# Kernel tuning notes

Measured on AMD Instinct MI355X. Metric: run time of the kernel, lower is better.

## Reference

```python
import jax, jax.numpy as jnp
import numpy as np

K = 20           # top_k
EPS_NORM = 1e-12  # F.normalize default eps


def setup_inputs() -> dict:
    key = jax.random.key(0)
    ks = jax.random.split(key, 16)
    B, C, R, S, SCB, ST, H = 8192, 3755, 214, 13, 30, 6, 64
    return {
        "char_logits": jax.random.normal(ks[0], (B, C), jnp.float32),
        "radical_logits": jax.random.normal(ks[1], (B, R), jnp.float32),
        "structure": jax.random.normal(ks[2], (B, S), jnp.float32),
        "stroke_count": jax.random.normal(ks[3], (B, SCB), jnp.float32),
        "stroke_types": jax.random.normal(ks[4], (B, ST), jnp.float32),
        "radical_mask": jax.random.randint(ks[5], (C, R), 0, 2, jnp.int32),
        "structure_label": jax.random.randint(ks[6], (C,), 0, S, jnp.int32),
        "stroke_count_label": jax.random.randint(ks[7], (C,), 0, SCB, jnp.int32),
        "stroke_type_sig": jax.random.uniform(ks[8], (C, ST), jnp.float32),
        "W1": jax.random.normal(ks[9], (6, H), jnp.float32) * 0.3,
        "b1": jax.random.normal(ks[10], (H,), jnp.float32) * 0.1,
        "W2": jax.random.normal(ks[11], (H, 1), jnp.float32) * 0.3,
        "b2": jax.random.normal(ks[12], (1,), jnp.float32) * 0.1,
        "reranker_weight": jnp.asarray(0.1, jnp.float32),
    }


def _features(char_logits, radical_logits, structure, stroke_count, stroke_types,
              radical_mask, structure_label, stroke_count_label, stroke_type_sig,
              top_idx):
    sg = jax.lax.stop_gradient
    # all model outputs except char_logits are detached by caller; char_logits
    # is detached inside _compute_features for the neural-confidence feature
    rl, st, sc, sty = sg(radical_logits), sg(structure), sg(stroke_count), sg(stroke_types)
    cl_d = sg(char_logits)

    # feature 1/2: radical match & false-alarm ratios
    radical_probs = jax.nn.sigmoid(rl)                              # (B, R)
    cand_mask = radical_mask[top_idx].astype(jnp.float32)           # (B, K, R)
    detected = jnp.einsum('br,bkr->bk', radical_probs, cand_mask)   # (B, K)
    cand_counts = jnp.maximum(cand_mask.sum(-1), 1.0)
    radical_match_ratio = detected / cand_counts
    total_prob = jnp.maximum(radical_probs.sum(-1, keepdims=True), 1e-6)  # (B,1)
    false_alarm_mass = radical_probs.sum(-1, keepdims=True) - detected
    radical_false_ratio = false_alarm_mass / total_prob

    # feature 3: structure match probability
    structure_probs = jax.nn.softmax(st, axis=-1)                   # (B, S)
    cand_structure = structure_label[top_idx]                       # (B, K)
    structure_match = jnp.take_along_axis(structure_probs, cand_structure, axis=1)

    # feature 4: normalized stroke-count distance
    stroke_pred = jnp.argmax(sc, axis=-1)                           # (B,)
    cand_stroke = stroke_count_label[top_idx]                       # (B, K)
    stroke_distance = jnp.abs(stroke_pred[:, None] - cand_stroke).astype(jnp.float32) / 29.0

    # feature 5: zero-masked stroke-type cosine
    cand_sig = stroke_type_sig[top_idx]                             # (B, K, 6)
    sig_norm_val = jnp.linalg.norm(cand_sig, axis=-1)               # (B, K)
    has_sig = (sig_norm_val > 1e-6).astype(jnp.float32)
    pred_norm = sty / jnp.maximum(jnp.linalg.norm(sty, axis=-1, keepdims=True), EPS_NORM)
    cand_adj = cand_sig + 1e-8 * (1.0 - has_sig)[..., None]
    cand_norm = cand_adj / jnp.maximum(jnp.linalg.norm(cand_adj, axis=-1, keepdims=True), EPS_NORM)
    stroke_type_cos = jnp.einsum('bd,bkd->bk', pred_norm, cand_norm) * has_sig

    # feature 6: detached neural confidence
    neural_probs = jax.nn.softmax(cl_d, axis=-1)                    # (B, C)
    neural_conf = jnp.take_along_axis(neural_probs, top_idx, axis=1)

    return jnp.stack([radical_match_ratio, radical_false_ratio, structure_match,
                      stroke_distance, stroke_type_cos, neural_conf], axis=-1)  # (B, K, 6)


def reference(char_logits, radical_logits, structure, stroke_count, stroke_types,
              radical_mask, structure_label, stroke_count_label, stroke_type_sig,
              W1, b1, W2, b2, reranker_weight):
    B = char_logits.shape[0]
    top_logits, top_idx = jax.lax.top_k(char_logits, K)             # (B, K)
    feats = _features(char_logits, radical_logits, structure, stroke_count,
                      stroke_types, radical_mask, structure_label,
                      stroke_count_label, stroke_type_sig, top_idx)
    h = jax.nn.relu(feats @ W1 + b1)                                # (B, K, H)
    rerank_scores = (h @ W2 + b2)[..., 0]                           # (B, K)
    combined_top = top_logits + reranker_weight * rerank_scores
    rows = jnp.arange(B)[:, None]
    return char_logits.at[rows, top_idx].set(combined_top)
```

## Files before the change

kernel.cpp:

```cpp
#include <hip/hip_runtime.h>
#include <math.h>

#define NB   8192
#define NC   3755
#define NR   214
#define NS   13
#define NSC  30
#define NST  6
#define NH   64
#define KTOP 20
#define RPB  4
#define NT   (RPB * 64)
#define NQT  15
#define NBIN 1024
#define CAP  192

__device__ __forceinline__ unsigned sortkey(float x) {
    unsigned u = __float_as_uint(x);
    return (u & 0x80000000u) ? ~u : (u | 0x80000000u);
}
__device__ __forceinline__ float inv_sortkey(unsigned k) {
    unsigned u = (k & 0x80000000u) ? (k ^ 0x80000000u) : ~k;
    return __uint_as_float(u);
}

__global__ __launch_bounds__(NT, 8) void select_kernel(
    const float* __restrict__ char_logits,
    float*       __restrict__ out,
    float*       __restrict__ ws_topv,
    int*         __restrict__ ws_topi,
    float*       __restrict__ ws_stat)
{
    const int tid  = threadIdx.x;
    const int lane = tid & 63;
    const int wave = tid >> 6;
    const int row  = blockIdx.x * RPB + wave;

    __shared__ unsigned           s_hist32[RPB / 2][NBIN];
    __shared__ unsigned long long s_cand[RPB][CAP];
    __shared__ int s_cnt[RPB];
    __shared__ int s_need[RPB];

    const int      hw  = wave >> 1;
    const unsigned hsh = (wave & 1) * 16;

    const size_t rowOff = (size_t)row * NC;
    const float* __restrict__ rin  = char_logits + rowOff;
    float*       __restrict__ rout = out + rowOff;

    const int a     = (int)((4 - (rowOff & 3)) & 3);
    const int nq    = (NC - a) >> 2;
    const int ntail = NC - a - 4 * nq;

    int ext_idx = -1;
    if (lane < a)                           ext_idx = lane;
    else if (lane >= 8 && lane < 8 + ntail) ext_idx = a + 4 * nq + (lane - 8);

    for (int i = tid; i < (RPB / 2) * NBIN; i += NT)
        (&s_hist32[0][0])[i] = 0u;
    if (tid < RPB) s_cnt[tid] = 0;
    __syncthreads();

    const unsigned floork1 = 0xC0000000u;
    float m0 = -INFINITY, m1 = -INFINITY, m2 = -INFINITY, m3 = -INFINITY;
    float ext = -INFINITY;
    if (ext_idx >= 0) {
        ext = rin[ext_idx]; rout[ext_idx] = ext;
        unsigned k = sortkey(ext);
        if (k >= floork1) atomicAdd(&s_hist32[hw][k >> 22], 1u << hsh);
    }
    for (int t = 0; t < NQT; ++t) {
        int q = lane + t * 64;
        if (q < nq) {
            float4 x = *reinterpret_cast<const float4*>(rin + a + 4 * q);
            *reinterpret_cast<float4*>(rout + a + 4 * q) = x;
            m0 = fmaxf(m0, x.x); m1 = fmaxf(m1, x.y);
            m2 = fmaxf(m2, x.z); m3 = fmaxf(m3, x.w);
            unsigned k0 = sortkey(x.x), k1 = sortkey(x.y);
            unsigned k2 = sortkey(x.z), k3 = sortkey(x.w);
            if (k0 >= floork1) atomicAdd(&s_hist32[hw][k0 >> 22], 1u << hsh);
            if (k1 >= floork1) atomicAdd(&s_hist32[hw][k1 >> 22], 1u << hsh);
            if (k2 >= floork1) atomicAdd(&s_hist32[hw][k2 >> 22], 1u << hsh);
            if (k3 >= floork1) atomicAdd(&s_hist32[hw][k3 >> 22], 1u << hsh);
        }
    }
    float lmax = fmaxf(fmaxf(m0, m1), fmaxf(fmaxf(m2, m3), ext));
#pragma unroll
    for (int off = 32; off > 0; off >>= 1) lmax = fmaxf(lmax, __shfl_xor(lmax, off));
    const float rowmax = lmax;
    __syncthreads();

    int B0 = -1;
    {
        int bb = (int)(sortkey(rowmax) >> 22);
        int fb = (int)(floork1 >> 22);
        int cum = 0;
        while (bb >= fb) {
            cum += (int)((s_hist32[hw][bb] >> hsh) & 0xFFFFu);
            if (cum >= KTOP) break;
            --bb;
        }
        B0 = (cum >= KTOP) ? bb : -1;
    }
    const int need2 = (B0 < 0) ? 1 : 0;
    if (lane == 0) s_need[wave] = need2;
    __syncthreads();

    const int any2 = s_need[0] | s_need[1] | s_need[2] | s_need[3];
    if (any2) {
        if (need2) {
#pragma unroll
            for (int i = 0; i < NBIN / 64; ++i) s_hist32[hw][lane + i * 64] = 0u;
        }
        __syncthreads();
        if (need2) {
            for (int t = 0; t < NQT; ++t) {
                int q = lane + t * 64;
                if (q < nq) {
                    float4 x = *reinterpret_cast<const float4*>(rin + a + 4 * q);
                    atomicAdd(&s_hist32[hw][sortkey(x.x) >> 22], 1u << hsh);
                    atomicAdd(&s_hist32[hw][sortkey(x.y) >> 22], 1u << hsh);
                    atomicAdd(&s_hist32[hw][sortkey(x.z) >> 22], 1u << hsh);
                    atomicAdd(&s_hist32[hw][sortkey(x.w) >> 22], 1u << hsh);
                }
            }
            if (ext_idx >= 0) atomicAdd(&s_hist32[hw][sortkey(ext) >> 22], 1u << hsh);
        }
        __syncthreads();
        if (need2) {
            int bb = (int)(sortkey(rowmax) >> 22);
            int cum = 0;
            while (bb >= 0) {
                cum += (int)((s_hist32[hw][bb] >> hsh) & 0xFFFFu);
                if (cum >= KTOP) break;
                --bb;
            }
            B0 = bb;
        }
    }

    float e0 = 0.f, e1 = 0.f, e2 = 0.f, e3 = 0.f;
    if (ext_idx >= 0) {
        e0 = __expf(ext - rowmax);
        unsigned k = sortkey(ext);
        if ((int)(k >> 22) >= B0) {
            int pos = atomicAdd(&s_cnt[wave], 1);
            if (pos < CAP)
                s_cand[wave][pos] = ((unsigned long long)k << 32) | (0xFFFFFFFFu - (unsigned)ext_idx);
        }
    }
    for (int t = 0; t < NQT; ++t) {
        int q = lane + t * 64;
        if (q < nq) {
            float4 x = *reinterpret_cast<const float4*>(rin + a + 4 * q);
            e0 += __expf(x.x - rowmax);
            e1 += __expf(x.y - rowmax);
            e2 += __expf(x.z - rowmax);
            e3 += __expf(x.w - rowmax);
            unsigned kk[4] = { sortkey(x.x), sortkey(x.y), sortkey(x.z), sortkey(x.w) };
#pragma unroll
            for (int j = 0; j < 4; ++j) {
                if ((int)(kk[j] >> 22) >= B0) {
                    int pos = atomicAdd(&s_cnt[wave], 1);
                    if (pos < CAP)
                        s_cand[wave][pos] = ((unsigned long long)kk[j] << 32)
                                          | (0xFFFFFFFFu - (unsigned)(a + 4*q + j));
                }
            }
        }
    }
    float le = (e0 + e1) + (e2 + e3);
#pragma unroll
    for (int off = 32; off > 0; off >>= 1) le += __shfl_xor(le, off);
    __syncthreads();

    int M = s_cnt[wave]; if (M > CAP) M = CAP;

    for (int c = lane; c < M; c += 64) {
        unsigned long long pc = s_cand[wave][c];
        int rank = 0;
        for (int j = 0; j < M; ++j) rank += (s_cand[wave][j] > pc) ? 1 : 0;
        if (rank < KTOP) {
            ws_topv[(size_t)row * KTOP + rank] = inv_sortkey((unsigned)(pc >> 32));
            ws_topi[(size_t)row * KTOP + rank] = (int)(0xFFFFFFFFu - (unsigned)(pc & 0xFFFFFFFFu));
        }
    }
    if (lane == 0) {
        ws_stat[2 * row + 0] = rowmax;
        ws_stat[2 * row + 1] = le;
    }
}

__global__ __launch_bounds__(256, 8) void rerank_kernel(
    const float* __restrict__ radical_logits,
    const float* __restrict__ structure,
    const float* __restrict__ stroke_count,
    const float* __restrict__ stroke_types,
    const int*   __restrict__ radical_mask,
    const int*   __restrict__ structure_label,
    const int*   __restrict__ stroke_count_label,
    const float* __restrict__ stroke_type_sig,
    const float* __restrict__ W1,
    const float* __restrict__ b1,
    const float* __restrict__ W2,
    const float* __restrict__ b2,
    const float* __restrict__ rw,
    const float* __restrict__ ws_topv,
    const int*   __restrict__ ws_topi,
    const float* __restrict__ ws_stat,
    float*       __restrict__ out)
{
    const int row  = blockIdx.x;
    const int tid  = threadIdx.x;
    const int lane = tid & 63;
    const int wave = tid >> 6;

    __shared__ float s_probs[216];
    __shared__ float s_struct[NS];
    __shared__ float s_aux[8];
    __shared__ float s_topv[KTOP];
    __shared__ int   s_topi[KTOP];
    __shared__ float s_stat2[2];

    if (tid < NR)
        s_probs[tid] = 1.f / (1.f + __expf(-radical_logits[(size_t)row * NR + tid]));
    if (tid < KTOP) {
        s_topv[tid] = ws_topv[(size_t)row * KTOP + tid];
        s_topi[tid] = ws_topi[(size_t)row * KTOP + tid];
    }
    if (tid == 216) {
        float sv[NS]; float m = -INFINITY;
#pragma unroll
        for (int i = 0; i < NS; ++i) { sv[i] = structure[(size_t)row * NS + i]; m = fmaxf(m, sv[i]); }
        float s = 0.f;
#pragma unroll
        for (int i = 0; i < NS; ++i) { sv[i] = __expf(sv[i] - m); s += sv[i]; }
        float inv = 1.f / s;
#pragma unroll
        for (int i = 0; i < NS; ++i) s_struct[i] = sv[i] * inv;
    } else if (tid == 217) {
        float bv = -INFINITY; int bi = 0;
#pragma unroll
        for (int i = 0; i < NSC; ++i) {
            float x = stroke_count[(size_t)row * NSC + i];
            if (x > bv) { bv = x; bi = i; }
        }
        s_aux[6] = (float)bi;
    } else if (tid == 218) {
        float t6[NST]; float ss = 0.f;
#pragma unroll
        for (int i = 0; i < NST; ++i) { t6[i] = stroke_types[(size_t)row * NST + i]; ss += t6[i] * t6[i]; }
        float inv = 1.f / fmaxf(sqrtf(ss), 1e-12f);
#pragma unroll
        for (int i = 0; i < NST; ++i) s_aux[i] = t6[i] * inv;
    } else if (tid == 219) {
        s_stat2[0] = ws_stat[2 * row + 0];
        s_stat2[1] = ws_stat[2 * row + 1];
    }
    __syncthreads();

    float psum = 0.f;
#pragma unroll
    for (int i = 0; i < 4; ++i) {
        int r = lane + i * 64;
        if (r < NR) psum += s_probs[r];
    }
#pragma unroll
    for (int off = 32; off > 0; off >>= 1) psum += __shfl_xor(psum, off);
    const float total = psum;

    const float rowmax = s_stat2[0];
    const float sumexp = s_stat2[1];
    const float b1v = b1[lane];
    float w1v[6];
#pragma unroll
    for (int j = 0; j < 6; ++j) w1v[j] = W1[j * NH + lane];
    const float w2v = W2[lane];
    const float b2v = b2[0];
    const float wrk = rw[0];
    const float spred = s_aux[6];

#pragma unroll
    for (int j = 0; j < KTOP / 4; ++j) {
        const int   k  = wave * (KTOP / 4) + j;
        const int   ci = __builtin_amdgcn_readfirstlane(s_topi[k]);
        const float tv = s_topv[k];
        const int* __restrict__ mrow = radical_mask + (size_t)ci * NR;
        float det = 0.f, cnt = 0.f;
#pragma unroll
        for (int i = 0; i < 4; ++i) {
            int r = lane + i * 64;
            if (r < NR) {
                float m = (float)mrow[r];
                det += s_probs[r] * m;
                cnt += m;
            }
        }
#pragma unroll
        for (int off = 32; off > 0; off >>= 1) {
            det += __shfl_xor(det, off);
            cnt += __shfl_xor(cnt, off);
        }
        float f1 = det / fmaxf(cnt, 1.f);
        float f2 = (total - det) / fmaxf(total, 1e-6f);
        float f3 = s_struct[structure_label[ci]];
        float f4 = fabsf(spred - (float)stroke_count_label[ci]) * (1.f / 29.f);
        float sig[NST]; float ss = 0.f;
#pragma unroll
        for (int i = 0; i < NST; ++i) { sig[i] = stroke_type_sig[(size_t)ci * NST + i]; ss += sig[i] * sig[i]; }
        float nrm = sqrtf(ss);
        float has = (nrm > 1e-6f) ? 1.f : 0.f;
        float add = 1e-8f * (1.f - has);
        float ss2 = 0.f;
#pragma unroll
        for (int i = 0; i < NST; ++i) { sig[i] += add; ss2 += sig[i] * sig[i]; }
        float inv = 1.f / fmaxf(sqrtf(ss2), 1e-12f);
        float dot = 0.f;
#pragma unroll
        for (int i = 0; i < NST; ++i) dot += s_aux[i] * sig[i] * inv;
        float f5 = dot * has;
        float f6 = __expf(tv - rowmax) / sumexp;

        float acc = b1v + f1 * w1v[0] + f2 * w1v[1] + f3 * w1v[2]
                        + f4 * w1v[3] + f5 * w1v[4] + f6 * w1v[5];
        float h = fmaxf(acc, 0.f);
        float part = h * w2v;
#pragma unroll
        for (int off = 32; off > 0; off >>= 1) part += __shfl_xor(part, off);
        if (lane == 0) out[(size_t)row * NC + ci] = tv + wrk * (part + b2v);
    }
}

extern "C" void kernel_launch(void* const* d_in, const int* in_sizes, int n_in,
                              void* d_out, int out_size, void* d_ws, size_t ws_size,
                              hipStream_t stream) {
    (void)in_sizes; (void)n_in; (void)out_size; (void)ws_size;
    const float* char_logits        = (const float*)d_in[0];
    const float* radical_logits     = (const float*)d_in[1];
    const float* structure          = (const float*)d_in[2];
    const float* stroke_count       = (const float*)d_in[3];
    const float* stroke_types       = (const float*)d_in[4];
    const int*   radical_mask       = (const int*)d_in[5];
    const int*   structure_label    = (const int*)d_in[6];
    const int*   stroke_count_label = (const int*)d_in[7];
    const float* stroke_type_sig    = (const float*)d_in[8];
    const float* W1                 = (const float*)d_in[9];
    const float* b1                 = (const float*)d_in[10];
    const float* W2                 = (const float*)d_in[11];
    const float* b2                 = (const float*)d_in[12];
    const float* rw                 = (const float*)d_in[13];
    float* out = (float*)d_out;

    float* ws_topv = (float*)d_ws;
    int*   ws_topi = (int*)(ws_topv + (size_t)NB * KTOP);
    float* ws_stat = (float*)(ws_topi + (size_t)NB * KTOP);

    select_kernel<<<NB / RPB, NT, 0, stream>>>(char_logits, out, ws_topv, ws_topi, ws_stat);
    rerank_kernel<<<NB, 256, 0, stream>>>(
        radical_logits, structure, stroke_count, stroke_types,
        radical_mask, structure_label, stroke_count_label, stroke_type_sig,
        W1, b1, W2, b2, rw, ws_topv, ws_topi, ws_stat, out);
}
```

Measured before the change: 391.0 us.

## Collect top-k candidates and softmax sum in a single pass over each row

Replaces the histogram-then-second-pass scheme with one pass. That pass gathers candidates above a fixed threshold (values >= 2.0) directly into shared memory and accumulates an unshifted exp sum, which is rescaled by exp(-rowmax). A fallback path with a histogram and second pass runs only when the candidate count falls outside [K, CAP] or rowmax is large. This removes the histogram zeroing, the histogram atomics and the second read of the row in the common case. In exchange, the unshifted exp sum risks overflow or precision loss, and the fast path depends on the input distribution producing few values above the threshold.

```diff
diff --git a/kernel.cpp b/kernel.cpp
--- a/kernel.cpp
+++ b/kernel.cpp
@@ -56,64 +56,67 @@
     if (lane < a)                           ext_idx = lane;
     else if (lane >= 8 && lane < 8 + ntail) ext_idx = a + 4 * nq + (lane - 8);
 
-    for (int i = tid; i < (RPB / 2) * NBIN; i += NT)
-        (&s_hist32[0][0])[i] = 0u;
     if (tid < RPB) s_cnt[tid] = 0;
     __syncthreads();
 
-    const unsigned floork1 = 0xC0000000u;
+    const unsigned FLOORK = 0xC0000000u;
     float m0 = -INFINITY, m1 = -INFINITY, m2 = -INFINITY, m3 = -INFINITY;
+    float e0 = 0.f, e1 = 0.f, e2 = 0.f, e3 = 0.f;
     float ext = -INFINITY;
     if (ext_idx >= 0) {
         ext = rin[ext_idx]; rout[ext_idx] = ext;
+        e0 += __expf(ext);
+        m0 = fmaxf(m0, ext);
         unsigned k = sortkey(ext);
-        if (k >= floork1) atomicAdd(&s_hist32[hw][k >> 22], 1u << hsh);
+        if (k >= FLOORK) {
+            int pos = atomicAdd(&s_cnt[wave], 1);
+            if (pos < CAP)
+                s_cand[wave][pos] = ((unsigned long long)k << 32) | (0xFFFFFFFFu - (unsigned)ext_idx);
+        }
     }
     for (int t = 0; t < NQT; ++t) {
         int q = lane + t * 64;
         if (q < nq) {
             float4 x = *reinterpret_cast<const float4*>(rin + a + 4 * q);
             *reinterpret_cast<float4*>(rout + a + 4 * q) = x;
+            e0 += __expf(x.x); e1 += __expf(x.y);
+            e2 += __expf(x.z); e3 += __expf(x.w);
             m0 = fmaxf(m0, x.x); m1 = fmaxf(m1, x.y);
             m2 = fmaxf(m2, x.z); m3 = fmaxf(m3, x.w);
-            unsigned k0 = sortkey(x.x), k1 = sortkey(x.y);
-            unsigned k2 = sortkey(x.z), k3 = sortkey(x.w);
-            if (k0 >= floork1) atomicAdd(&s_hist32[hw][k0 >> 22], 1u << hsh);
-            if (k1 >= floork1) atomicAdd(&s_hist32[hw][k1 >> 22], 1u << hsh);
-            if (k2 >= floork1) atomicAdd(&s_hist32[hw][k2 >> 22], 1u << hsh);
-            if (k3 >= floork1) atomicAdd(&s_hist32[hw][k3 >> 22], 1u << hsh);
-        }
-    }
-    float lmax = fmaxf(fmaxf(m0, m1), fmaxf(fmaxf(m2, m3), ext));
+            unsigned kk[4] = { sortkey(x.x), sortkey(x.y), sortkey(x.z), sortkey(x.w) };
+#pragma unroll
+            for (int j = 0; j < 4; ++j) {
+                if (kk[j] >= FLOORK) {
+                    int pos = atomicAdd(&s_cnt[wave], 1);
+                    if (pos < CAP)
+                        s_cand[wave][pos] = ((unsigned long long)kk[j] << 32)
+                                          | (0xFFFFFFFFu - (unsigned)(a + 4*q + j));
+                }
+            }
+        }
+    }
+    float lmax = fmaxf(fmaxf(m0, m1), fmaxf(m2, m3));
 #pragma unroll
     for (int off = 32; off > 0; off >>= 1) lmax = fmaxf(lmax, __shfl_xor(lmax, off));
     const float rowmax = lmax;
+    float S = (e0 + e1) + (e2 + e3);
+#pragma unroll
+    for (int off = 32; off > 0; off >>= 1) S += __shfl_xor(S, off);
+
+    int M = s_cnt[wave];
+    const bool ok = (M >= KTOP) && (M <= CAP) && (fabsf(rowmax) <= 60.f);
+    float sumexp = S * __expf(-rowmax);
+    if (lane == 0) s_need[wave] = ok ? 0 : 1;
     __syncthreads();
-
-    int B0 = -1;
-    {
-        int bb = (int)(sortkey(rowmax) >> 22);
-        int fb = (int)(floork1 >> 22);
-        int cum = 0;
-        while (bb >= fb) {
-            cum += (int)((s_hist32[hw][bb] >> hsh) & 0xFFFFu);
-            if (cum >= KTOP) break;
-            --bb;
-        }
-        B0 = (cum >= KTOP) ? bb : -1;
-    }
-    const int need2 = (B0 < 0) ? 1 : 0;
-    if (lane == 0) s_need[wave] = need2;
-    __syncthreads();
-
-    const int any2 = s_need[0] | s_need[1] | s_need[2] | s_need[3];
-    if (any2) {
-        if (need2) {
-#pragma unroll
-            for (int i = 0; i < NBIN / 64; ++i) s_hist32[hw][lane + i * 64] = 0u;
-        }
+    const int any = s_need[0] | s_need[1] | s_need[2] | s_need[3];
+
+    if (any) {
+        const bool bad = !ok;
+        for (int i = tid; i < (RPB / 2) * NBIN; i += NT)
+            (&s_hist32[0][0])[i] = 0u;
         __syncthreads();
-        if (need2) {
+        if (bad) {
+            if (ext_idx >= 0) atomicAdd(&s_hist32[hw][sortkey(ext) >> 22], 1u << hsh);
             for (int t = 0; t < NQT; ++t) {
                 int q = lane + t * 64;
                 if (q < nq) {
@@ -124,57 +127,56 @@
                     atomicAdd(&s_hist32[hw][sortkey(x.w) >> 22], 1u << hsh);
                 }
             }
-            if (ext_idx >= 0) atomicAdd(&s_hist32[hw][sortkey(ext) >> 22], 1u << hsh);
         }
         __syncthreads();
-        if (need2) {
-            int bb = (int)(sortkey(rowmax) >> 22);
-            int cum = 0;
+        int B0 = 0;
+        if (bad) {
+            int bb = (int)(sortkey(rowmax) >> 22), cum = 0;
             while (bb >= 0) {
                 cum += (int)((s_hist32[hw][bb] >> hsh) & 0xFFFFu);
                 if (cum >= KTOP) break;
                 --bb;
             }
-            B0 = bb;
-        }
-    }
-
-    float e0 = 0.f, e1 = 0.f, e2 = 0.f, e3 = 0.f;
-    if (ext_idx >= 0) {
-        e0 = __expf(ext - rowmax);
-        unsigned k = sortkey(ext);
-        if ((int)(k >> 22) >= B0) {
-            int pos = atomicAdd(&s_cnt[wave], 1);
-            if (pos < CAP)
-                s_cand[wave][pos] = ((unsigned long long)k << 32) | (0xFFFFFFFFu - (unsigned)ext_idx);
-        }
-    }
-    for (int t = 0; t < NQT; ++t) {
-        int q = lane + t * 64;
-        if (q < nq) {
-            float4 x = *reinterpret_cast<const float4*>(rin + a + 4 * q);
-            e0 += __expf(x.x - rowmax);
-            e1 += __expf(x.y - rowmax);
-            e2 += __expf(x.z - rowmax);
-            e3 += __expf(x.w - rowmax);
-            unsigned kk[4] = { sortkey(x.x), sortkey(x.y), sortkey(x.z), sortkey(x.w) };
-#pragma unroll
-            for (int j = 0; j < 4; ++j) {
-                if ((int)(kk[j] >> 22) >= B0) {
+            B0 = (bb < 0) ? 0 : bb;
+            if (lane == 0) s_cnt[wave] = 0;
+        }
+        __syncthreads();
+        if (bad) {
+            float f0 = 0.f, f1 = 0.f, f2 = 0.f, f3 = 0.f;
+            if (ext_idx >= 0) {
+                f0 += __expf(ext - rowmax);
+                unsigned k = sortkey(ext);
+                if ((int)(k >> 22) >= B0) {
                     int pos = atomicAdd(&s_cnt[wave], 1);
                     if (pos < CAP)
-                        s_cand[wave][pos] = ((unsigned long long)kk[j] << 32)
-                                          | (0xFFFFFFFFu - (unsigned)(a + 4*q + j));
+                        s_cand[wave][pos] = ((unsigned long long)k << 32) | (0xFFFFFFFFu - (unsigned)ext_idx);
                 }
             }
-        }
-    }
-    float le = (e0 + e1) + (e2 + e3);
-#pragma unroll
-    for (int off = 32; off > 0; off >>= 1) le += __shfl_xor(le, off);
-    __syncthreads();
-
-    int M = s_cnt[wave]; if (M > CAP) M = CAP;
+            for (int t = 0; t < NQT; ++t) {
+                int q = lane + t * 64;
+                if (q < nq) {
+                    float4 x = *reinterpret_cast<const float4*>(rin + a + 4 * q);
+                    f0 += __expf(x.x - rowmax); f1 += __expf(x.y - rowmax);
+                    f2 += __expf(x.z - rowmax); f3 += __expf(x.w - rowmax);
+                    unsigned kk[4] = { sortkey(x.x), sortkey(x.y), sortkey(x.z), sortkey(x.w) };
+#pragma unroll
+                    for (int j = 0; j < 4; ++j) {
+                        if ((int)(kk[j] >> 22) >= B0) {
+                            int pos = atomicAdd(&s_cnt[wave], 1);
+                            if (pos < CAP)
+                                s_cand[wave][pos] = ((unsigned long long)kk[j] << 32)
+                                                  | (0xFFFFFFFFu - (unsigned)(a + 4*q + j));
+                        }
+                    }
+                }
+            }
+            float ls = (f0 + f1) + (f2 + f3);
+#pragma unroll
+            for (int off = 32; off > 0; off >>= 1) ls += __shfl_xor(ls, off);
+            sumexp = ls;
+            M = s_cnt[wave]; if (M > CAP) M = CAP;
+        }
+    }
 
     for (int c = lane; c < M; c += 64) {
         unsigned long long pc = s_cand[wave][c];
@@ -187,7 +189,7 @@
     }
     if (lane == 0) {
         ws_stat[2 * row + 0] = rowmax;
-        ws_stat[2 * row + 1] = le;
+        ws_stat[2 * row + 1] = sumexp;
     }
 }
 
```

After: 343.7 us. 1.14x faster.
